# Performance work log

Measured on AMD Instinct MI355X. Metric: run time of the kernel, lower is better.

The kernel has to match this reference:

```python
import jax
import jax.numpy as jnp
import numpy as np

# --- dimensions ---
N, B, E, T = 16384, 64, 262144, 1048576   # atoms, molecules, edges, triplets
R, S = 128, 7                              # num_radial, num_spherical
A, EM, TR = 128, 256, 32                   # emb_size_atom, emb_size_edge, emb_size_trip
CRBF, C, BIL, L = 16, 16, 64, 2            # emb_size_rbf, emb_size_cbf, emb_size_bil_trip, num_blocks
NKR, DP = 128, 8                           # num_k_rbf, downprojection_size
CUTOFF, K_CUT, DK = 6.0, 0.4, 0.2


def _k_grid_np():
    ax = np.arange(-2, 3) * DK
    g = np.stack(np.meshgrid(ax, ax, ax, indexing='ij'), -1).reshape(-1, 3)
    nrm = np.linalg.norm(g, axis=1)
    return g[(nrm <= K_CUT + 1e-9) & (nrm > 1e-12)].astype(np.float32)  # [32,3]


def _k_rbf_np(kg):
    nrm = np.linalg.norm(kg, axis=1, keepdims=True)
    centers = np.linspace(0.0, K_CUT, NKR)[None, :]
    gamma = (NKR / K_CUT) ** 2
    return np.exp(-gamma * (nrm - centers) ** 2).astype(np.float32)  # [32,NKR]


def setup_inputs():
    key = jax.random.key(0)
    ks = iter(jax.random.split(key, 48))
    def nrm(shape, fan_in):
        return jax.random.normal(next(ks), shape, jnp.float32) * (fan_in ** -0.5)
    kg_np = _k_grid_np()
    apm = N // B  # atoms per molecule
    mol = jax.random.randint(next(ks), (E,), 0, B)
    inp = {
        'pos': jax.random.uniform(next(ks), (N, 3), jnp.float32) * 5.0,
        'atom_table': jax.random.normal(next(ks), (83, A), jnp.float32),
        'W_edge': nrm((2 * A + R, EM), 2 * A + R), 'b_edge': jnp.zeros((EM,), jnp.float32),
        'W_rbf3': nrm((R, CRBF), R), 'W_rbf3_E': nrm((L, CRBF, EM), CRBF),
        'W_cbf3': nrm((S, R, C), R),
        'W_ba': nrm((L, EM, EM), EM),
        'W_downtrip': nrm((L, EM, TR), EM),
        'W_bil': nrm((L, C, TR, BIL), C * TR),
        'W_up': nrm((L, BIL, EM), BIL),
        'W_res1': nrm((L, EM, EM), EM), 'W_res2': nrm((L, EM, EM), EM),
        'W_rbf_h': nrm((R, CRBF), R), 'W_h': nrm((L, CRBF, EM), CRBF),
        'W_atom': nrm((L, EM, A), EM),
        'k_grid': jnp.asarray(kg_np), 'k_rbf_values': jnp.asarray(_k_rbf_np(kg_np)),
        'W_downk': nrm((NKR, DP), NKR), 'W_kfilter': nrm((DP, A), DP),
        'W_ew': nrm((L, A, A), A),
        'W_cat': nrm((L, 2 * A + EM, EM), 2 * A + EM),
        'W_rbf_out': nrm((R, CRBF), R), 'W_oute': nrm((CRBF, EM), CRBF),
        'W_out1': nrm((EM, A), EM), 'W_out2': nrm((A, 1), A),
        'z': jax.random.randint(next(ks), (N,), 0, 83),
        'edge_src': mol * apm + jax.random.randint(next(ks), (E,), 0, apm),
        'edge_tgt': mol * apm + jax.random.randint(next(ks), (E,), 0, apm),
        'id3_ba': jax.random.randint(next(ks), (T,), 0, E),
        'id3_ca': jax.random.randint(next(ks), (T,), 0, E),
        'batch_idx': jnp.arange(N, dtype=jnp.int32) // apm,
    }
    return inp


def _legendre(x):
    # P_0..P_{S-1}(x) via recurrence
    p = [jnp.ones_like(x), x]
    for l in range(1, S - 1):
        p.append(((2 * l + 1) * x * p[-1] - l * p[-2]) / (l + 1))
    return jnp.stack(p[:S], axis=-1)  # [T,S]


def _forward(pos, atom_table, W_edge, b_edge, W_rbf3, W_rbf3_E, W_cbf3, W_ba,
             W_downtrip, W_bil, W_up, W_res1, W_res2, W_rbf_h, W_h, W_atom,
             k_grid, k_rbf_values, W_downk, W_kfilter, W_ew, W_cat,
             W_rbf_out, W_oute, W_out1, W_out2,
             z, edge_src, edge_tgt, id3_ba, id3_ca, batch_idx):
    seg = lambda x, ids, n: jax.ops.segment_sum(x, ids, num_segments=n)
    silu = jax.nn.silu
    isq2 = 2.0 ** -0.5

    # radial basis (spherical Bessel) with polynomial envelope p=5
    vec = pos[edge_src] - pos[edge_tgt]                       # [E,3]
    d = jnp.sqrt(jnp.sum(vec * vec, -1) + 1e-12)              # [E]
    ds = d / CUTOFF
    env = jnp.where(ds < 1.0, 1.0 - 21.0 * ds**5 + 35.0 * ds**6 - 15.0 * ds**7, 0.0)
    freq = jnp.arange(1, R + 1, dtype=pos.dtype) * jnp.pi
    rbf = env[:, None] * (2.0 / CUTOFF) ** 0.5 * jnp.sin(freq * ds[:, None]) / d[:, None]  # [E,R]

    # circular basis: Legendre polys of triplet angle b->a<-c, combined with rbf of edge c->a
    cos_ang = jnp.clip(jnp.sum(vec[id3_ba] * vec[id3_ca], -1) / (d[id3_ba] * d[id3_ca]), -1.0, 1.0)
    sph = _legendre(cos_ang)                                  # [T,S]
    rW = jnp.einsum('er,src->esc', rbf, W_cbf3)               # [E,S,C]
    cbf = jnp.zeros((sph.shape[0], C), pos.dtype)
    for s in range(S):  # small fixed loop over spherical order (memory-safe gather)
        cbf = cbf + sph[:, s, None] * rW[:, s, :][id3_ca]     # [T,C]

    # atom + edge embeddings
    h = atom_table[z]                                         # [N,A]
    m = silu(jnp.concatenate([h[edge_src], h[edge_tgt], rbf], -1) @ W_edge + b_edge)  # [E,EM]

    # Ewald k-space geometry and learned filter
    kdot = pos @ k_grid.T                                     # [N,K]
    cosk, sink = jnp.cos(kdot), jnp.sin(kdot)
    kf = silu(k_rbf_values @ W_downk) @ W_kfilter             # [K,A]

    for l in range(L):
        # triplet message passing: gather - bilinear with cbf - scatter
        rbf3e = (rbf @ W_rbf3) @ W_rbf3_E[l]                  # [E,EM]
        x_trip = silu((silu(m @ W_ba[l]) * rbf3e) @ W_downtrip[l])  # [E,TR]
        x_kj = x_trip[id3_ba]                                 # [T,TR]
        x3 = jnp.zeros((m.shape[0], BIL), m.dtype)
        for c in range(C):  # efficient bilinear, one cbf channel at a time
            x3 = x3 + seg(cbf[:, c, None] * x_kj, id3_ca, m.shape[0]) @ W_bil[l, c]
        m = (m + silu(x3 @ W_up[l])) * isq2
        m = (m + silu(silu(m @ W_res1[l]) @ W_res2[l])) * isq2
        # atom update: rbf-gated edge->atom scatter
        ha = seg(m * ((rbf @ W_rbf_h) @ W_h[l]), edge_tgt, h.shape[0]) @ W_atom[l]  # [N,A]
        # Ewald block: per-molecule structure factors, filtered in k-space
        sf_re = seg(cosk[:, :, None] * h[:, None, :], batch_idx, B) * kf  # [B,K,A]
        sf_im = seg(sink[:, :, None] * h[:, None, :], batch_idx, B) * kf
        ew = (jnp.einsum('nk,nka->na', cosk, sf_re[batch_idx]) +
              jnp.einsum('nk,nka->na', sink, sf_im[batch_idx]))           # [N,A]
        h = (h + silu(ha) + silu(ew @ W_ew[l])) * (3.0 ** -0.5)
        # edge refresh (concat block)
        m = silu(jnp.concatenate([h[edge_src], h[edge_tgt], m], -1) @ W_cat[l])

    # output block: rbf-gated scatter to atoms, per-molecule extensive energy
    Ea = seg(m * ((rbf @ W_rbf_out) @ W_oute), edge_tgt, h.shape[0])       # [N,EM]
    atom_e = silu(Ea @ W_out1) @ W_out2                                     # [N,1]
    return seg(atom_e[:, 0], batch_idx, B)                                  # [B]


def reference(pos, atom_table, W_edge, b_edge, W_rbf3, W_rbf3_E, W_cbf3, W_ba,
              W_downtrip, W_bil, W_up, W_res1, W_res2, W_rbf_h, W_h, W_atom,
              k_grid, k_rbf_values, W_downk, W_kfilter, W_ew, W_cat,
              W_rbf_out, W_oute, W_out1, W_out2,
              z, edge_src, edge_tgt, id3_ba, id3_ca, batch_idx):
    return _forward(pos, atom_table, W_edge, b_edge, W_rbf3, W_rbf3_E, W_cbf3, W_ba,
                    W_downtrip, W_bil, W_up, W_res1, W_res2, W_rbf_h, W_h, W_atom,
                    k_grid, k_rbf_values, W_downk, W_kfilter, W_ew, W_cat,
                    W_rbf_out, W_oute, W_out1, W_out2,
                    z, edge_src, edge_tgt, id3_ba, id3_ca, batch_idx)
```

## Files before the change

kernel.cpp:

```cpp
#include <hip/hip_runtime.h>
#include <math.h>

#define NA 16384
#define NB 64
#define NE 262144
#define NT 1048576
#define NR 128
#define DA 128
#define DEM 256
#define DTR 32
#define DC 16
#define DBIL 64
#define DNKR 128
#define DDP 8
#define NK 32
#define APM 256
#define PI_F 3.14159265358979323846f

typedef unsigned short u16;
typedef unsigned int u32;
typedef __attribute__((ext_vector_type(8))) short bf16x8;
typedef __attribute__((ext_vector_type(4))) float f32x4;

__device__ __forceinline__ float silu_f(float x){ return x / (1.0f + __expf(-x)); }
__device__ __forceinline__ float us2f(u32 u){ return __uint_as_float(u<<16); }
__device__ __forceinline__ u16 f2us(float f){
  u32 x = __float_as_uint(f);
  u32 r = x + 0x7fffu + ((x>>16)&1u);
  return (u16)(r>>16);
}
__device__ __forceinline__ void unp8(uint4 v, float* o){
  o[0]=us2f(v.x&0xffffu); o[1]=us2f(v.x>>16);
  o[2]=us2f(v.y&0xffffu); o[3]=us2f(v.y>>16);
  o[4]=us2f(v.z&0xffffu); o[5]=us2f(v.z>>16);
  o[6]=us2f(v.w&0xffffu); o[7]=us2f(v.w>>16);
}
__device__ __forceinline__ uint4 pack8(const float* v){
  uint4 r;
  r.x = (u32)f2us(v[0]) | ((u32)f2us(v[1])<<16);
  r.y = (u32)f2us(v[2]) | ((u32)f2us(v[3])<<16);
  r.z = (u32)f2us(v[4]) | ((u32)f2us(v[5])<<16);
  r.w = (u32)f2us(v[6]) | ((u32)f2us(v[7])<<16);
  return r;
}
__device__ __forceinline__ float rbf_val(float d, int r){
  float ds = d*(1.0f/6.0f);
  float env = 0.0f;
  if (ds < 1.0f){
    float p2 = ds*ds, p5 = p2*p2*ds;
    env = 1.0f - 21.0f*p5 + 35.0f*p5*ds - 15.0f*p5*p2;
  }
  return env * 0.5773502691896258f * __sinf((float)(r+1)*PI_F*ds) / d;
}

__device__ __forceinline__ bf16x8 ldsA(const u16* sA, int row, int KLD, int slot){
  int s = slot ^ (row&7);
  return *(const bf16x8*)(sA + row*KLD + s*8);
}
__device__ __forceinline__ void stSlot(u16* sA, int row, int KLD, int slot, uint4 v){
  int s = slot ^ (row&7);
  *(uint4*)(sA + row*KLD + s*8) = v;
}
__device__ __forceinline__ void stW(u16* sA, int row, int KLD, int col, u16 v){
  int s = (col>>3) ^ (row&7);
  sA[row*KLD + s*8 + (col&7)] = v;
}
__device__ __forceinline__ bf16x8 ldB(const u16* Wt, int col, int K, int koff){
  return *(const bf16x8*)(Wt + (size_t)col*K + koff);
}

__global__ void k_zero(int* __restrict__ p, int n){
  int i = blockIdx.x*256+threadIdx.x; if (i<n) p[i]=0;
}

__global__ void k_wprep(const float* __restrict__ src, u16* __restrict__ dst,
                        int K, int N, int Kpad){
  int i = blockIdx.x*256+threadIdx.x;
  if (i >= N*Kpad) return;
  int n = i / Kpad, k = i - n*Kpad;
  dst[(size_t)n*Kpad + k] = (k<K)? f2us(src[(size_t)k*N + n]) : (u16)0;
}
__global__ void k_wprep_cbf(const float* __restrict__ src, u16* __restrict__ dst){
  int i = blockIdx.x*256+threadIdx.x;
  if (i >= 112*128) return;
  int n = i>>7, k = i&127;
  int s = n>>4, c = n&15;
  dst[i] = f2us(src[s*2048 + k*16 + c]);
}

__global__ void k_geom(const float* __restrict__ pos, const int* __restrict__ src,
                       const int* __restrict__ tgt, float4* __restrict__ vecd,
                       float* __restrict__ dlen){
  int e = blockIdx.x*256+threadIdx.x;
  if (e >= NE) return;
  int s = src[e], t = tgt[e];
  float vx = pos[s*3+0]-pos[t*3+0];
  float vy = pos[s*3+1]-pos[t*3+1];
  float vz = pos[s*3+2]-pos[t*3+2];
  float d = sqrtf(vx*vx+vy*vy+vz*vz + 1e-12f);
  vecd[e] = make_float4(vx,vy,vz,1.0f/d);
  dlen[e] = d;
}

__global__ void __launch_bounds__(256)
k_rbf16(const float* __restrict__ dlen, const float* __restrict__ W1,
        const float* __restrict__ W2, const float* __restrict__ W3,
        u16* __restrict__ r16a, u16* __restrict__ r16h, u16* __restrict__ r16o){
  __shared__ float rb[4*128];
  int e0 = blockIdx.x*4;
  int tid = threadIdx.x, eg = tid>>6, lt = tid&63;
  int e = e0+eg;
  float d = dlen[e];
  rb[eg*128+lt]    = rbf_val(d, lt);
  rb[eg*128+lt+64] = rbf_val(d, lt+64);
  __syncthreads();
  if (lt < 48){
    int which = lt>>4, jj = lt&15;
    const float* W = (which==0)? W1 : (which==1)? W2 : W3;
    float acc=0.f;
    for (int r=0;r<NR;r++) acc += rb[eg*128+r]*W[r*16+jj];
    u16* o = (which==0)? r16a : (which==1)? r16h : r16o;
    o[(size_t)e*16+jj] = f2us(acc);
  }
}

__global__ void k_gather_h(const float* __restrict__ table, const int* __restrict__ z,
                           float* __restrict__ h){
  int idx = blockIdx.x*256 + threadIdx.x;
  int n = idx >> 7, a = idx & 127;
  h[idx] = table[z[n]*DA + a];
}

__global__ void k_kdot(const float* __restrict__ pos, const float* __restrict__ kg,
                       float* __restrict__ cosk, float* __restrict__ sink_){
  int idx = blockIdx.x*256+threadIdx.x;
  int n = idx>>5, k = idx&31;
  float dotv = pos[n*3]*kg[k*3]+pos[n*3+1]*kg[k*3+1]+pos[n*3+2]*kg[k*3+2];
  float s, c;
  sincosf(dotv, &s, &c);
  cosk[idx] = c; sink_[idx] = s;
}

__global__ void k_kf(const float* __restrict__ krbf, const float* __restrict__ Wd,
                     const float* __restrict__ Wf, float* __restrict__ kf){
  __shared__ float t[NK*DDP];
  int tid = threadIdx.x;
  { int k = tid>>3, d = tid&7;
    float s=0.f;
    for (int r=0;r<DNKR;r++) s += krbf[k*DNKR+r]*Wd[r*DDP+d];
    t[tid] = silu_f(s); }
  __syncthreads();
  for (int idx=tid; idx<NK*DA; idx+=256){
    int k = idx>>7, a = idx&127;
    float s=0.f;
    #pragma unroll
    for (int d=0; d<DDP; d++) s += t[k*DDP+d]*Wf[d*DA+a];
    kf[idx]=s;
  }
}

__global__ void k_count(const int* __restrict__ ids, int num, int* __restrict__ cnt){
  int i = blockIdx.x*256+threadIdx.x;
  if (i<num) atomicAdd(&cnt[ids[i]],1);
}
__global__ void k_scan1(const int* __restrict__ cnt, int n, int* __restrict__ loc,
                        int* __restrict__ part){
  __shared__ int lds[256];
  int i = blockIdx.x*256+threadIdx.x;
  int v = (i<n)?cnt[i]:0;
  lds[threadIdx.x]=v; __syncthreads();
  for (int off=1; off<256; off<<=1){
    int tv = (threadIdx.x >= (unsigned)off)? lds[threadIdx.x-off]:0;
    __syncthreads();
    lds[threadIdx.x]+=tv;
    __syncthreads();
  }
  if (i<n) loc[i] = lds[threadIdx.x]-v;
  if (threadIdx.x==255) part[blockIdx.x]=lds[255];
}
__global__ void k_scan2(int* __restrict__ part, int nparts){
  __shared__ int lds[1024];
  int tid=threadIdx.x;
  for (int i=tid;i<1024;i+=256) lds[i] = (i<nparts)? part[i] : 0;
  __syncthreads();
  if (tid==0){
    int run=0;
    for (int i=0;i<nparts;i++){ int v=lds[i]; lds[i]=run; run+=v; }
  }
  __syncthreads();
  for (int i=tid;i<1024;i+=256) if (i<nparts) part[i]=lds[i];
}
__global__ void k_scan3(const int* __restrict__ loc, const int* __restrict__ part,
                        const int* __restrict__ cnt, int n, int* __restrict__ off){
  int i = blockIdx.x*256+threadIdx.x;
  if (i<n){ int o = loc[i]+part[i>>8]; off[i]=o; if (i==n-1) off[n]=o+cnt[i]; }
}
__global__ void k_copy_int(const int* __restrict__ a, int n, int* __restrict__ b){
  int i=blockIdx.x*256+threadIdx.x; if(i<n) b[i]=a[i];
}
__global__ void k_fill(const int* __restrict__ ids, int num, int* __restrict__ cur,
                       int* __restrict__ list){
  int i = blockIdx.x*256+threadIdx.x;
  if (i<num){ int p = atomicAdd(&cur[ids[i]],1); list[p]=i; }
}
__global__ void k_fill_val(const int* __restrict__ ids, const int* __restrict__ vals,
                           int num, int* __restrict__ cur, int* __restrict__ list){
  int i = blockIdx.x*256+threadIdx.x;
  if (i<num){ int p = atomicAdd(&cur[ids[i]],1); list[p]=vals[i]; }
}


__global__ void __launch_bounds__(256)
k_edgeinit_mx(const float* __restrict__ h, const float* __restrict__ dlen,
              const u16* __restrict__ Wt, const float* __restrict__ bias,
              const int* __restrict__ src, const int* __restrict__ tgt,
              u16* __restrict__ outm){
  __shared__ u16 sA[64*256];
  int e0 = blockIdx.x*64;
  int j = threadIdx.x, lane = j&63, w = j>>6;
  int rbase = (w&1)*32, cbase = (w>>1)*128;
  int l15 = lane&15, kg = lane>>4;
  f32x4 acc[2][8];
  #pragma unroll
  for (int rt=0;rt<2;rt++)
    #pragma unroll
    for (int i=0;i<8;i++) acc[rt][i] = (f32x4){0.f,0.f,0.f,0.f};
  for (int idx=j; idx<64*32; idx+=256){
    int row = idx>>5, slot = idx&31;
    int e = e0+row;
    const float* srcp = (slot<16)? (h + (size_t)src[e]*DA + slot*8)
                                 : (h + (size_t)tgt[e]*DA + (slot-16)*8);
    float v[8];
    float4 q0 = *(const float4*)srcp, q1 = *(const float4*)(srcp+4);
    v[0]=q0.x; v[1]=q0.y; v[2]=q0.z; v[3]=q0.w;
    v[4]=q1.x; v[5]=q1.y; v[6]=q1.z; v[7]=q1.w;
    stSlot(sA, row, 256, slot, pack8(v));
  }
  __syncthreads();
  #pragma unroll 2
  for (int kc=0; kc<8; kc++){
    bf16x8 a0 = ldsA(sA, rbase+l15,    256, kc*4+kg);
    bf16x8 a1 = ldsA(sA, rbase+16+l15, 256, kc*4+kg);
    #pragma unroll
    for (int ct=0; ct<8; ct++){
      bf16x8 b = ldB(Wt, cbase+ct*16+l15, 384, kc*32+kg*8);
      acc[0][ct] = __builtin_amdgcn_mfma_f32_16x16x32_bf16(a0, b, acc[0][ct], 0,0,0);
      acc[1][ct] = __builtin_amdgcn_mfma_f32_16x16x32_bf16(a1, b, acc[1][ct], 0,0,0);
    }
  }
  __syncthreads();
  for (int idx=j; idx<64*16; idx+=256){
    int row = idx>>4, slot = idx&15;
    float dv = dlen[e0+row];
    float v[8];
    #pragma unroll
    for (int q=0;q<8;q++) v[q] = rbf_val(dv, slot*8+q);
    stSlot(sA, row, 256, slot, pack8(v));
  }
  __syncthreads();
  #pragma unroll 2
  for (int kc=8; kc<12; kc++){
    bf16x8 a0 = ldsA(sA, rbase+l15,    256, (kc-8)*4+kg);
    bf16x8 a1 = ldsA(sA, rbase+16+l15, 256, (kc-8)*4+kg);
    #pragma unroll
    for (int ct=0; ct<8; ct++){
      bf16x8 b = ldB(Wt, cbase+ct*16+l15, 384, kc*32+kg*8);
      acc[0][ct] = __builtin_amdgcn_mfma_f32_16x16x32_bf16(a0, b, acc[0][ct], 0,0,0);
      acc[1][ct] = __builtin_amdgcn_mfma_f32_16x16x32_bf16(a1, b, acc[1][ct], 0,0,0);
    }
  }
  #pragma unroll
  for (int rt=0;rt<2;rt++)
  #pragma unroll
  for (int ct=0; ct<8; ct++){
    int col = cbase + ct*16 + l15;
    float bv = bias[col];
    #pragma unroll
    for (int r=0;r<4;r++){
      int row = rbase + rt*16 + kg*4 + r;
      outm[(size_t)(e0+row)*DEM + col] = f2us(silu_f(acc[rt][ct][r] + bv));
    }
  }
}

__global__ void __launch_bounds__(256)
k_ba_dt_mx(const u16* __restrict__ m, const u16* __restrict__ WtBA,
           const u16* __restrict__ r16, const u16* __restrict__ WtR3E,
           const u16* __restrict__ WtDT, u16* __restrict__ xtrip){
  __shared__ u16 sM[32*256];
  __shared__ u16 sR[32*64];
  int e0 = blockIdx.x*32;
  int j = threadIdx.x, lane = j&63, w = j>>6;
  for (int p=j; p<32*32; p+=256){
    int row = p>>5, slot = p&31;
    uint4 v = *(const uint4*)(m + (size_t)(e0+row)*DEM + slot*8);
    stSlot(sM, row, 256, slot, v);
  }
  for (int p=j; p<32*8; p+=256){
    int row = p>>3, slot = p&7;
    uint4 v = {0u,0u,0u,0u};
    if (slot<2) v = *(const uint4*)(r16 + (size_t)(e0+row)*16 + slot*8);
    stSlot(sR, row, 64, slot, v);
  }
  __syncthreads();
  int rbase = (w&1)*16, cbase = (w>>1)*128;
  int l15 = lane&15, kg = lane>>4;
  int arow = rbase + l15;
  f32x4 accA[8], accG[8];
  #pragma unroll
  for (int i=0;i<8;i++){ accA[i]=(f32x4){0.f,0.f,0.f,0.f}; accG[i]=(f32x4){0.f,0.f,0.f,0.f}; }
  #pragma unroll 2
  for (int kc=0; kc<8; kc++){
    bf16x8 a = ldsA(sM, arow, 256, kc*4+kg);
    #pragma unroll
    for (int ct=0; ct<8; ct++){
      bf16x8 b = ldB(WtBA, cbase+ct*16+l15, 256, kc*32+kg*8);
      accA[ct] = __builtin_amdgcn_mfma_f32_16x16x32_bf16(a, b, accA[ct], 0,0,0);
    }
  }
  { bf16x8 a = ldsA(sR, arow, 64, kg);
    #pragma unroll
    for (int ct=0; ct<8; ct++){
      bf16x8 b = ldB(WtR3E, cbase+ct*16+l15, 32, kg*8);
      accG[ct] = __builtin_amdgcn_mfma_f32_16x16x32_bf16(a, b, accG[ct], 0,0,0);
    } }
  __syncthreads();
  #pragma unroll
  for (int ct=0; ct<8; ct++){
    int col = cbase + ct*16 + l15;
    #pragma unroll
    for (int r=0;r<4;r++){
      int row = rbase + kg*4 + r;
      stW(sM, row, 256, col, f2us(silu_f(accA[ct][r])*accG[ct][r]));
    }
  }
  __syncthreads();
  int rb2 = (w&1)*16, ct2 = (w>>1);
  int arow2 = rb2 + l15;
  f32x4 acc2 = (f32x4){0.f,0.f,0.f,0.f};
  #pragma unroll 2
  for (int kc=0; kc<8; kc++){
    bf16x8 a = ldsA(sM, arow2, 256, kc*4+kg);
    bf16x8 b = ldB(WtDT, ct2*16+l15, 256, kc*32+kg*8);
    acc2 = __builtin_amdgcn_mfma_f32_16x16x32_bf16(a, b, acc2, 0,0,0);
  }
  #pragma unroll
  for (int r=0;r<4;r++){
    int row = rb2 + kg*4 + r;
    int col = ct2*16 + l15;
    xtrip[(size_t)(e0+row)*DTR + col] = f2us(silu_f(acc2[r]));
  }
}

__global__ void __launch_bounds__(256)
k_trip(const int* __restrict__ ca_off, const int* __restrict__ ba_list,
       const float4* __restrict__ vecd, const float* __restrict__ dlen,
       const u16* __restrict__ WtCBF, const u16* __restrict__ xtrip,
       const u16* __restrict__ WtBIL, const u16* __restrict__ WtUP,
       u16* __restrict__ m){
  __shared__ u16 sS3[16*512];
  __shared__ u16 sRB[16*128];
  __shared__ float rWl[16*112];
  __shared__ u16 sX3[16*64];
  int e0 = blockIdx.x*16;
  int tid = threadIdx.x, lane = tid&63, w = tid>>6;
  int l15 = lane&15, kg = lane>>4;
  for (int idx=tid; idx<2048; idx+=256){
    int e = idx>>7, r = idx&127;
    stW(sRB, e, 128, r, f2us(rbf_val(dlen[e0+e], r)));
  }
  __syncthreads();
  for (int ct=w; ct<7; ct+=4){
    f32x4 acc = (f32x4){0.f,0.f,0.f,0.f};
    for (int kc=0; kc<4; kc++){
      bf16x8 a = ldsA(sRB, l15, 128, kc*4+kg);
      bf16x8 b = ldB(WtCBF, ct*16+l15, 128, kc*32+kg*8);
      acc = __builtin_amdgcn_mfma_f32_16x16x32_bf16(a, b, acc, 0,0,0);
    }
    #pragma unroll
    for (int r=0;r<4;r++)
      rWl[(kg*4+r)*112 + ct*16 + l15] = acc[r];
  }
  __syncthreads();
  int half = lane>>5, tr = lane&31;
  for (int sub=0; sub<4; sub++){
    int el = w*4+sub, e = e0+el;
    float4 vd = vecd[e];
    float a0=0.f,a1=0.f,a2=0.f,a3=0.f,a4=0.f,a5=0.f,a6=0.f;
    int beg = ca_off[e], end = ca_off[e+1];
    int cnt = end - beg;
    int c0 = (cnt+1)>>1;
    int mybeg = beg + half*c0;
    int myend = half ? end : beg+c0;
    float4 bd = make_float4(0.f,0.f,0.f,1.f);
    float xk = 0.f;
    if (mybeg<myend){
      int b0 = ba_list[mybeg];
      bd = vecd[b0];
      xk = us2f(xtrip[(size_t)b0*DTR + tr]);
    }
    for (int ti=mybeg; ti<myend; ti++){
      int bn = (ti+1<myend)? ba_list[ti+1] : 0;
      float4 bd_n = vecd[bn];
      float xk_n = us2f(xtrip[(size_t)bn*DTR + tr]);
      float x = (vd.x*bd.x + vd.y*bd.y + vd.z*bd.z)*vd.w*bd.w;
      x = fminf(1.0f, fmaxf(-1.0f, x));
      float p2 = (3.f*x*x - 1.f)*0.5f;
      float p3 = (5.f*x*p2 - 2.f*x)*(1.0f/3.0f);
      float p4 = (7.f*x*p3 - 3.f*p2)*0.25f;
      float p5 = (9.f*x*p4 - 4.f*p3)*0.2f;
      float p6 = (11.f*x*p5 - 5.f*p4)*(1.0f/6.0f);
      a0 += xk;    a1 += x*xk;  a2 += p2*xk; a3 += p3*xk;
      a4 += p4*xk; a5 += p5*xk; a6 += p6*xk;
      bd = bd_n; xk = xk_n;
    }
    a0 += __shfl_xor(a0, 32); a1 += __shfl_xor(a1, 32);
    a2 += __shfl_xor(a2, 32); a3 += __shfl_xor(a3, 32);
    a4 += __shfl_xor(a4, 32); a5 += __shfl_xor(a5, 32);
    a6 += __shfl_xor(a6, 32);
    const float* rwe = rWl + el*112;
    #pragma unroll
    for (int q=0;q<8;q++){
      int c = half*8+q;
      float s3 = rwe[c]*a0 + rwe[16+c]*a1 + rwe[32+c]*a2 + rwe[48+c]*a3
               + rwe[64+c]*a4 + rwe[80+c]*a5 + rwe[96+c]*a6;
      stW(sS3, el, 512, c*32+tr, f2us(s3));
    }
  }
  __syncthreads();
  { f32x4 acc = (f32x4){0.f,0.f,0.f,0.f};
    #pragma unroll 2
    for (int kc=0; kc<16; kc++){
      bf16x8 a = ldsA(sS3, l15, 512, kc*4+kg);
      bf16x8 b = ldB(WtBIL, w*16+l15, 512, kc*32+kg*8);
      acc = __builtin_amdgcn_mfma_f32_16x16x32_bf16(a, b, acc, 0,0,0);
    }
    #pragma unroll
    for (int r=0;r<4;r++)
      stW(sX3, kg*4+r, 64, w*16+l15, f2us(acc[r]));
  }
  __syncthreads();
  f32x4 acc2[4];
  #pragma unroll
  for (int i=0;i<4;i++) acc2[i] = (f32x4){0.f,0.f,0.f,0.f};
  for (int kc=0; kc<2; kc++){
    bf16x8 a = ldsA(sX3, l15, 64, kc*4+kg);
    #pragma unroll
    for (int ct=0; ct<4; ct++){
      bf16x8 b = ldB(WtUP, w*64+ct*16+l15, 64, kc*32+kg*8);
      acc2[ct] = __builtin_amdgcn_mfma_f32_16x16x32_bf16(a, b, acc2[ct], 0,0,0);
    }
  }
  #pragma unroll
  for (int ct=0; ct<4; ct++){
    int col = w*64 + ct*16 + l15;
    #pragma unroll
    for (int r=0;r<4;r++){
      int row = kg*4 + r;
      size_t oi = (size_t)(e0+row)*DEM + col;
      m[oi] = f2us((us2f(m[oi]) + silu_f(acc2[ct][r]))*0.7071067811865476f);
    }
  }
}

__global__ void __launch_bounds__(256)
k_res_mx(const u16* __restrict__ WtR1, const u16* __restrict__ WtR2, u16* __restrict__ m){
  __shared__ u16 sM[64*256];
  int e0 = blockIdx.x*64;
  int j = threadIdx.x, lane = j&63, w = j>>6;
  for (int p=j; p<64*32; p+=256){
    int row = p>>5, slot = p&31;
    uint4 v = *(const uint4*)(m + (size_t)(e0+row)*DEM + slot*8);
    stSlot(sM, row, 256, slot, v);
  }
  __syncthreads();
  int rbase = (w&1)*32, cbase = (w>>1)*128;
  int l15 = lane&15, kg = lane>>4;
  f32x4 acc[2][8];
  #pragma unroll
  for (int rt=0;rt<2;rt++)
    #pragma unroll
    for (int i=0;i<8;i++) acc[rt][i]=(f32x4){0.f,0.f,0.f,0.f};
  #pragma unroll 2
  for (int kc=0; kc<8; kc++){
    bf16x8 a0 = ldsA(sM, rbase+l15,    256, kc*4+kg);
    bf16x8 a1 = ldsA(sM, rbase+16+l15, 256, kc*4+kg);
    #pragma unroll
    for (int ct=0; ct<8; ct++){
      bf16x8 b = ldB(WtR1, cbase+ct*16+l15, 256, kc*32+kg*8);
      acc[0][ct] = __builtin_amdgcn_mfma_f32_16x16x32_bf16(a0, b, acc[0][ct], 0,0,0);
      acc[1][ct] = __builtin_amdgcn_mfma_f32_16x16x32_bf16(a1, b, acc[1][ct], 0,0,0);
    }
  }
  __syncthreads();
  #pragma unroll
  for (int rt=0;rt<2;rt++)
  #pragma unroll
  for (int ct=0; ct<8; ct++){
    int col = cbase + ct*16 + l15;
    #pragma unroll
    for (int r=0;r<4;r++)
      stW(sM, rbase + rt*16 + kg*4 + r, 256, col, f2us(silu_f(acc[rt][ct][r])));
  }
  __syncthreads();
  #pragma unroll
  for (int rt=0;rt<2;rt++)
    #pragma unroll
    for (int i=0;i<8;i++) acc[rt][i]=(f32x4){0.f,0.f,0.f,0.f};
  #pragma unroll 2
  for (int kc=0; kc<8; kc++){
    bf16x8 a0 = ldsA(sM, rbase+l15,    256, kc*4+kg);
    bf16x8 a1 = ldsA(sM, rbase+16+l15, 256, kc*4+kg);
    #pragma unroll
    for (int ct=0; ct<8; ct++){
      bf16x8 b = ldB(WtR2, cbase+ct*16+l15, 256, kc*32+kg*8);
      acc[0][ct] = __builtin_amdgcn_mfma_f32_16x16x32_bf16(a0, b, acc[0][ct], 0,0,0);
      acc[1][ct] = __builtin_amdgcn_mfma_f32_16x16x32_bf16(a1, b, acc[1][ct], 0,0,0);
    }
  }
  #pragma unroll
  for (int rt=0;rt<2;rt++)
  #pragma unroll
  for (int ct=0; ct<8; ct++){
    int col = cbase + ct*16 + l15;
    #pragma unroll
    for (int r=0;r<4;r++){
      int row = rbase + rt*16 + kg*4 + r;
      size_t oi = (size_t)(e0+row)*DEM + col;
      float orig = us2f(m[oi]);
      m[oi] = f2us((orig + silu_f(acc[rt][ct][r]))*0.7071067811865476f);
    }
  }
}

__global__ void __launch_bounds__(256)
k_catref_mx(const float* __restrict__ h, const u16* __restrict__ Wt,
            const int* __restrict__ src, const int* __restrict__ tgt,
            u16* __restrict__ m){
  __shared__ u16 sA[64*256];
  int e0 = blockIdx.x*64;
  int j = threadIdx.x, lane = j&63, w = j>>6;
  int rbase = (w&1)*32, cbase = (w>>1)*128;
  int l15 = lane&15, kg = lane>>4;
  f32x4 acc[2][8];
  #pragma unroll
  for (int rt=0;rt<2;rt++)
    #pragma unroll
    for (int i=0;i<8;i++) acc[rt][i]=(f32x4){0.f,0.f,0.f,0.f};
  for (int idx=j; idx<64*32; idx+=256){
    int row = idx>>5, slot = idx&31;
    int e = e0+row;
    const float* srcp = (slot<16)? (h + (size_t)src[e]*DA + slot*8)
                                 : (h + (size_t)tgt[e]*DA + (slot-16)*8);
    float v[8];
    float4 q0 = *(const float4*)srcp, q1 = *(const float4*)(srcp+4);
    v[0]=q0.x; v[1]=q0.y; v[2]=q0.z; v[3]=q0.w;
    v[4]=q1.x; v[5]=q1.y; v[6]=q1.z; v[7]=q1.w;
    stSlot(sA, row, 256, slot, pack8(v));
  }
  __syncthreads();
  #pragma unroll 2
  for (int kc=0; kc<8; kc++){
    bf16x8 a0 = ldsA(sA, rbase+l15,    256, kc*4+kg);
    bf16x8 a1 = ldsA(sA, rbase+16+l15, 256, kc*4+kg);
    #pragma unroll
    for (int ct=0; ct<8; ct++){
      bf16x8 b = ldB(Wt, cbase+ct*16+l15, 512, kc*32+kg*8);
      acc[0][ct] = __builtin_amdgcn_mfma_f32_16x16x32_bf16(a0, b, acc[0][ct], 0,0,0);
      acc[1][ct] = __builtin_amdgcn_mfma_f32_16x16x32_bf16(a1, b, acc[1][ct], 0,0,0);
    }
  }
  __syncthreads();
  for (int p=j; p<64*32; p+=256){
    int row = p>>5, slot = p&31;
    uint4 v = *(const uint4*)(m + (size_t)(e0+row)*DEM + slot*8);
    stSlot(sA, row, 256, slot, v);
  }
  __syncthreads();
  #pragma unroll 2
  for (int kc=8; kc<16; kc++){
    bf16x8 a0 = ldsA(sA, rbase+l15,    256, (kc-8)*4+kg);
    bf16x8 a1 = ldsA(sA, rbase+16+l15, 256, (kc-8)*4+kg);
    #pragma unroll
    for (int ct=0; ct<8; ct++){
      bf16x8 b = ldB(Wt, cbase+ct*16+l15, 512, kc*32+kg*8);
      acc[0][ct] = __builtin_amdgcn_mfma_f32_16x16x32_bf16(a0, b, acc[0][ct], 0,0,0);
      acc[1][ct] = __builtin_amdgcn_mfma_f32_16x16x32_bf16(a1, b, acc[1][ct], 0,0,0);
    }
  }
  __syncthreads();
  #pragma unroll
  for (int rt=0;rt<2;rt++)
  #pragma unroll
  for (int ct=0; ct<8; ct++){
    int col = cbase + ct*16 + l15;
    #pragma unroll
    for (int r=0;r<4;r++){
      int row = rbase + rt*16 + kg*4 + r;
      m[(size_t)(e0+row)*DEM + col] = f2us(silu_f(acc[rt][ct][r]));
    }
  }
}

__global__ void __launch_bounds__(256)
k_gseg(const int* __restrict__ off, const int* __restrict__ list,
       const u16* __restrict__ m, const u16* __restrict__ r16,
       const float* __restrict__ Wg, float* __restrict__ outp){
  __shared__ float sW[16*256];
  int n = blockIdx.x, j = threadIdx.x;
  for (int idx=j; idx<4096; idx+=256) sW[idx] = Wg[idx];
  __syncthreads();
  float s = 0.f;
  int beg = off[n], end = off[n+1];
  for (int ii=beg; ii<end; ii++){
    int e = list[ii];
    const uint4* rp = (const uint4*)(r16 + (size_t)e*16);
    float rv[16];
    unp8(rp[0], rv); unp8(rp[1], rv+8);
    float g = 0.f;
    #pragma unroll
    for (int i=0;i<16;i++) g += rv[i]*sW[i*256+j];
    s += us2f(m[(size_t)e*DEM + j])*g;
  }
  outp[(size_t)n*DEM + j] = s;
}

__global__ void k_sf(const float* __restrict__ cosk, const float* __restrict__ sink_,
                     const float* __restrict__ h, const float* __restrict__ kf,
                     float* __restrict__ sfre, float* __restrict__ sfim){
  int bk = blockIdx.x; int b = bk>>5, k = bk&31;
  int a = threadIdx.x;
  float sre=0.f, sim=0.f;
  int n0 = b*APM;
  for (int i=0;i<APM;i++){
    float c = cosk[(n0+i)*NK+k];
    float s = sink_[(n0+i)*NK+k];
    float hv = h[(size_t)(n0+i)*DA+a];
    sre += c*hv; sim += s*hv;
  }
  float f = kf[k*DA+a];
  sfre[(size_t)bk*DA+a] = sre*f;
  sfim[(size_t)bk*DA+a] = sim*f;
}

__global__ void k_ew(const float* __restrict__ cosk, const float* __restrict__ sink_,
                     const float* __restrict__ sfre, const float* __restrict__ sfim,
                     float* __restrict__ ew){
  int n = blockIdx.x; int a = threadIdx.x; int b = n>>8;
  float s=0.f;
  for (int k=0;k<NK;k++){
    s += cosk[n*NK+k]*sfre[(size_t)(b*NK+k)*DA+a] + sink_[n*NK+k]*sfim[(size_t)(b*NK+k)*DA+a];
  }
  ew[(size_t)n*DA+a]=s;
}

__global__ void __launch_bounds__(128)
k_hup(const float* __restrict__ hsum, const float* __restrict__ ewb,
      const float* __restrict__ Wat, const float* __restrict__ Wew,
      float* __restrict__ h){
  __shared__ float sA[16*256];
  __shared__ float sB[16*128];
  int row0 = blockIdx.x*16;
  int j = threadIdx.x;
  for (int idx=j; idx<4096; idx+=128) sA[idx] = hsum[(size_t)row0*DEM + idx];
  for (int idx=j; idx<2048; idx+=128) sB[idx] = ewb[(size_t)row0*DA + idx];
  __syncthreads();
  float a1[16], a2[16];
  #pragma unroll
  for (int i=0;i<16;i++){ a1[i]=0.f; a2[i]=0.f; }
  for (int k=0;k<256;k++){
    float w = Wat[k*DA+j];
    #pragma unroll
    for (int i=0;i<16;i++) a1[i] += sA[i*256+k]*w;
  }
  for (int k=0;k<128;k++){
    float w = Wew[k*DA+j];
    #pragma unroll
    for (int i=0;i<16;i++) a2[i] += sB[i*128+k]*w;
  }
  #pragma unroll
  for (int i=0;i<16;i++){
    size_t oi = (size_t)(row0+i)*DA + j;
    h[oi] = (h[oi] + silu_f(a1[i]) + silu_f(a2[i]))*0.5773502691896258f;
  }
}

__global__ void k_out_atom(const float* __restrict__ Ea, const float* __restrict__ W1,
                           const float* __restrict__ W2, float* __restrict__ atom_e){
  __shared__ float red[128];
  int n = blockIdx.x; int j = threadIdx.x;
  const float* row = Ea + (size_t)n*DEM;
  float s=0.f;
  for (int k=0;k<DEM;k++) s += row[k]*W1[k*DA+j];
  float v = silu_f(s)*W2[j];
  red[j]=v; __syncthreads();
  for (int st=64; st>0; st>>=1){ if (j<st) red[j]+=red[j+st]; __syncthreads(); }
  if (j==0) atom_e[n]=red[0];
}

__global__ void k_out_mol(const float* __restrict__ atom_e, float* __restrict__ out){
  __shared__ float red[256];
  int b = blockIdx.x; int t = threadIdx.x;
  red[t] = atom_e[b*APM+t]; __syncthreads();
  for (int st=128; st>0; st>>=1){ if (t<st) red[t]+=red[t+st]; __syncthreads(); }
  if (t==0) out[b]=red[0];
}

extern "C" void kernel_launch(void* const* d_in, const int* in_sizes, int n_in,
                              void* d_out, int out_size, void* d_ws, size_t ws_size,
                              hipStream_t stream){
  (void)in_sizes; (void)n_in; (void)out_size;
  const float* pos    = (const float*)d_in[0];
  const float* atab   = (const float*)d_in[1];
  const float* W_edge = (const float*)d_in[2];
  const float* b_edge = (const float*)d_in[3];
  const float* W_rbf3 = (const float*)d_in[4];
  const float* W_rbf3E= (const float*)d_in[5];
  const float* W_cbf3 = (const float*)d_in[6];
  const float* W_ba   = (const float*)d_in[7];
  const float* W_dt   = (const float*)d_in[8];
  const float* W_bil  = (const float*)d_in[9];
  const float* W_up   = (const float*)d_in[10];
  const float* W_r1   = (const float*)d_in[11];
  const float* W_r2   = (const float*)d_in[12];
  const float* W_rbfh = (const float*)d_in[13];
  const float* W_h    = (const float*)d_in[14];
  const float* W_atom = (const float*)d_in[15];
  const float* kgrid  = (const float*)d_in[16];
  const float* krbfv  = (const float*)d_in[17];
  const float* W_dk   = (const float*)d_in[18];
  const float* W_kf   = (const float*)d_in[19];
  const float* W_ewm  = (const float*)d_in[20];
  const float* W_cat  = (const float*)d_in[21];
  const float* W_rbfo = (const float*)d_in[22];
  const float* W_oute = (const float*)d_in[23];
  const float* W_o1   = (const float*)d_in[24];
  const float* W_o2   = (const float*)d_in[25];
  const int* z     = (const int*)d_in[26];
  const int* esrc  = (const int*)d_in[27];
  const int* etgt  = (const int*)d_in[28];
  const int* id3ba = (const int*)d_in[29];
  const int* id3ca = (const int*)d_in[30];
  float* out = (float*)d_out;

  char* base = (char*)d_ws;
  size_t off = 0;
  auto alloc = [&](size_t bytes)->char*{
    char* p = base + off;
    off += (bytes + 255) & ~(size_t)255;
    return p;
  };
  u16*   m     = (u16*)  alloc((size_t)NE*DEM*2);
  float4* vecd = (float4*)alloc((size_t)NE*16);
  float* dlen  = (float*)alloc((size_t)NE*4);
  u16*   r16a  = (u16*)  alloc((size_t)NE*16*2);
  u16*   r16h  = (u16*)  alloc((size_t)NE*16*2);
  u16*   r16o  = (u16*)  alloc((size_t)NE*16*2);
  float* h     = (float*)alloc((size_t)NA*DA*4);
  float* cosk  = (float*)alloc((size_t)NA*NK*4);
  float* sinkb = (float*)alloc((size_t)NA*NK*4);
  float* sfre  = (float*)alloc((size_t)NB*NK*DA*4);
  float* sfim  = (float*)alloc((size_t)NB*NK*DA*4);
  float* kf    = (float*)alloc((size_t)NK*DA*4);
  float* atome = (float*)alloc((size_t)NA*4);
  char*  scr   = alloc((size_t)24*1024*1024);
  int* tgt_off = (int*)alloc((size_t)(NA+1)*4);
  int* tgt_list= (int*)alloc((size_t)NE*4);
  int* ca_off  = (int*)alloc((size_t)(NE+1)*4);
  int* ca_list = (int*)alloc((size_t)NT*4);
  int* parts   = (int*)alloc((size_t)1024*4);
  u16* wt_edge = (u16*)alloc((size_t)256*384*2);
  u16* wt_ba   = (u16*)alloc((size_t)2*256*256*2);
  u16* wt_r3e  = (u16*)alloc((size_t)2*256*32*2);
  u16* wt_dt   = (u16*)alloc((size_t)2*32*256*2);
  u16* wt_up   = (u16*)alloc((size_t)2*256*64*2);
  u16* wt_r1   = (u16*)alloc((size_t)2*256*256*2);
  u16* wt_r2   = (u16*)alloc((size_t)2*256*256*2);
  u16* wt_cat  = (u16*)alloc((size_t)2*256*512*2);
  u16* wt_cbf  = (u16*)alloc((size_t)112*128*2);
  u16* wt_bil  = (u16*)alloc((size_t)2*64*512*2);
  size_t need = off;
  if (ws_size < need) return;

  u16*   xtrip = (u16*)scr;
  float* hsum  = (float*)scr;
  float* ewb   = (float*)(scr + (size_t)16*1024*1024);
  int* tmpi    = (int*)r16a;
  int* tgt_cnt = tmpi;
  int* tgt_loc = tmpi + NA;
  int* tgt_cur = tmpi + 2*NA;
  int* ca_cnt  = tmpi + 3*NA;
  int* ca_loc  = ca_cnt + NE;
  int* ca_cur  = ca_loc + NE;

  auto wprep = [&](const float* src, u16* dst, int K, int N, int Kpad){
    int tot = N*Kpad;
    k_wprep<<<(tot+255)/256, 256, 0, stream>>>(src, dst, K, N, Kpad);
  };
  wprep(W_edge, wt_edge, 384, 256, 384);
  k_wprep_cbf<<<(112*128+255)/256, 256, 0, stream>>>(W_cbf3, wt_cbf);
  for (int l=0; l<2; l++){
    wprep(W_ba  + (size_t)l*256*256, wt_ba  + (size_t)l*256*256, 256, 256, 256);
    wprep(W_rbf3E+(size_t)l*16*256,  wt_r3e + (size_t)l*256*32,  16,  256, 32);
    wprep(W_dt  + (size_t)l*256*32,  wt_dt  + (size_t)l*32*256,  256, 32,  256);
    wprep(W_up  + (size_t)l*64*256,  wt_up  + (size_t)l*256*64,  64,  256, 64);
    wprep(W_r1  + (size_t)l*256*256, wt_r1  + (size_t)l*256*256, 256, 256, 256);
    wprep(W_r2  + (size_t)l*256*256, wt_r2  + (size_t)l*256*256, 256, 256, 256);
    wprep(W_cat + (size_t)l*512*256, wt_cat + (size_t)l*256*512, 512, 256, 512);
    wprep(W_bil + (size_t)l*512*64,  wt_bil + (size_t)l*64*512,  512, 64,  512);
  }

  k_geom<<<NE/256, 256, 0, stream>>>(pos, esrc, etgt, vecd, dlen);

  k_zero<<<NA/256, 256, 0, stream>>>(tgt_cnt, NA);
  k_count<<<NE/256, 256, 0, stream>>>(etgt, NE, tgt_cnt);
  k_scan1<<<NA/256, 256, 0, stream>>>(tgt_cnt, NA, tgt_loc, parts);
  k_scan2<<<1, 256, 0, stream>>>(parts, NA/256);
  k_scan3<<<NA/256, 256, 0, stream>>>(tgt_loc, parts, tgt_cnt, NA, tgt_off);
  k_copy_int<<<NA/256, 256, 0, stream>>>(tgt_off, NA, tgt_cur);
  k_fill<<<NE/256, 256, 0, stream>>>(etgt, NE, tgt_cur, tgt_list);

  k_zero<<<NE/256, 256, 0, stream>>>(ca_cnt, NE);
  k_count<<<NT/256, 256, 0, stream>>>(id3ca, NT, ca_cnt);
  k_scan1<<<NE/256, 256, 0, stream>>>(ca_cnt, NE, ca_loc, parts);
  k_scan2<<<1, 256, 0, stream>>>(parts, NE/256);
  k_scan3<<<NE/256, 256, 0, stream>>>(ca_loc, parts, ca_cnt, NE, ca_off);
  k_copy_int<<<NE/256, 256, 0, stream>>>(ca_off, NE, ca_cur);
  k_fill_val<<<NT/256, 256, 0, stream>>>(id3ca, id3ba, NT, ca_cur, ca_list);

  k_rbf16<<<NE/4, 256, 0, stream>>>(dlen, W_rbf3, W_rbfh, W_rbfo, r16a, r16h, r16o);
  k_gather_h<<<NA*DA/256, 256, 0, stream>>>(atab, z, h);
  k_kdot<<<NA*NK/256, 256, 0, stream>>>(pos, kgrid, cosk, sinkb);
  k_kf<<<1, 256, 0, stream>>>(krbfv, W_dk, W_kf, kf);
  k_edgeinit_mx<<<NE/64, 256, 0, stream>>>(h, dlen, wt_edge, b_edge, esrc, etgt, m);

  for (int l=0; l<2; l++){
    k_ba_dt_mx<<<NE/32, 256, 0, stream>>>(m, wt_ba + (size_t)l*256*256,
                                          r16a, wt_r3e + (size_t)l*256*32,
                                          wt_dt + (size_t)l*32*256, xtrip);
    k_trip<<<NE/16, 256, 0, stream>>>(ca_off, ca_list, vecd, dlen, wt_cbf,
                                      xtrip, wt_bil + (size_t)l*64*512,
                                      wt_up + (size_t)l*256*64, m);
    k_res_mx<<<NE/64, 256, 0, stream>>>(wt_r1 + (size_t)l*256*256,
                                        wt_r2 + (size_t)l*256*256, m);
    k_gseg<<<NA, 256, 0, stream>>>(tgt_off, tgt_list, m, r16h, W_h + (size_t)l*16*DEM, hsum);
    k_sf<<<NB*NK, 128, 0, stream>>>(cosk, sinkb, h, kf, sfre, sfim);
    k_ew<<<NA, 128, 0, stream>>>(cosk, sinkb, sfre, sfim, ewb);
    k_hup<<<NA/16, 128, 0, stream>>>(hsum, ewb, W_atom + (size_t)l*DEM*DA,
                                     W_ewm + (size_t)l*DA*DA, h);
    k_catref_mx<<<NE/64, 256, 0, stream>>>(h, wt_cat + (size_t)l*256*512, esrc, etgt, m);
  }

  k_gseg<<<NA, 256, 0, stream>>>(tgt_off, tgt_list, m, r16o, W_oute, hsum);
  k_out_atom<<<NA, 128, 0, stream>>>(hsum, W_o1, W_o2, atome);
  k_out_mol<<<NB, 256, 0, stream>>>(atome, out);
}
```

Before: 3.891 ms.

## Renumber edges in target-sorted order so segment reductions read contiguously

Edges are permuted into target-sorted order using the tgt CSR list. Triplet indices are remapped through an inverse permutation, and all per-edge arrays are built in that order. This lets the per-atom segment sums read m and rbf rows contiguously instead of gathering through an index list, which should improve locality in k_gseg and in the triplet and catref gathers. The cost is a few extra preprocessing kernels. Edge ordering now depends on the atomic fill order, but the sums are order-invariant.

```diff
diff --git a/kernel.cpp b/kernel.cpp
--- a/kernel.cpp
+++ b/kernel.cpp
@@ -88,6 +88,28 @@
   dst[i] = f2us(src[s*2048 + k*16 + c]);
 }
 
+__global__ void k_iperm(const int* __restrict__ list, int n, int* __restrict__ iperm){
+  int i = blockIdx.x*256+threadIdx.x;
+  if (i<n) iperm[list[i]] = i;
+}
+__global__ void k_permute2(const int* __restrict__ list, const int* __restrict__ a,
+                           const int* __restrict__ b, int n,
+                           int* __restrict__ ap, int* __restrict__ bp){
+  int i = blockIdx.x*256+threadIdx.x;
+  if (i<n){ int e = list[i]; ap[i]=a[e]; bp[i]=b[e]; }
+}
+__global__ void k_count_map(const int* __restrict__ ids, const int* __restrict__ map,
+                            int num, int* __restrict__ cnt){
+  int i = blockIdx.x*256+threadIdx.x;
+  if (i<num) atomicAdd(&cnt[map[ids[i]]],1);
+}
+__global__ void k_fill_valmap(const int* __restrict__ ids, const int* __restrict__ vals,
+                              const int* __restrict__ map, int num,
+                              int* __restrict__ cur, int* __restrict__ list){
+  int i = blockIdx.x*256+threadIdx.x;
+  if (i<num){ int p = atomicAdd(&cur[map[ids[i]]],1); list[p]=map[vals[i]]; }
+}
+
 __global__ void k_geom(const float* __restrict__ pos, const int* __restrict__ src,
                        const int* __restrict__ tgt, float4* __restrict__ vecd,
                        float* __restrict__ dlen){
@@ -202,11 +224,6 @@
                        int* __restrict__ list){
   int i = blockIdx.x*256+threadIdx.x;
   if (i<num){ int p = atomicAdd(&cur[ids[i]],1); list[p]=i; }
-}
-__global__ void k_fill_val(const int* __restrict__ ids, const int* __restrict__ vals,
-                           int num, int* __restrict__ cur, int* __restrict__ list){
-  int i = blockIdx.x*256+threadIdx.x;
-  if (i<num){ int p = atomicAdd(&cur[ids[i]],1); list[p]=vals[i]; }
 }
 
 
@@ -603,17 +620,16 @@
 }
 
 __global__ void __launch_bounds__(256)
-k_gseg(const int* __restrict__ off, const int* __restrict__ list,
-       const u16* __restrict__ m, const u16* __restrict__ r16,
-       const float* __restrict__ Wg, float* __restrict__ outp){
+k_gseg_seq(const int* __restrict__ off, const u16* __restrict__ m,
+           const u16* __restrict__ r16, const float* __restrict__ Wg,
+           float* __restrict__ outp){
   __shared__ float sW[16*256];
   int n = blockIdx.x, j = threadIdx.x;
   for (int idx=j; idx<4096; idx+=256) sW[idx] = Wg[idx];
   __syncthreads();
   float s = 0.f;
   int beg = off[n], end = off[n+1];
-  for (int ii=beg; ii<end; ii++){
-    int e = list[ii];
+  for (int e=beg; e<end; e++){
     const uint4* rp = (const uint4*)(r16 + (size_t)e*16);
     float rv[16];
     unp8(rp[0], rv); unp8(rp[1], rv+8);
@@ -766,6 +782,9 @@
   char*  scr   = alloc((size_t)24*1024*1024);
   int* tgt_off = (int*)alloc((size_t)(NA+1)*4);
   int* tgt_list= (int*)alloc((size_t)NE*4);
+  int* iperm   = (int*)alloc((size_t)NE*4);
+  int* esrc_p  = (int*)alloc((size_t)NE*4);
+  int* etgt_p  = (int*)alloc((size_t)NE*4);
   int* ca_off  = (int*)alloc((size_t)(NE+1)*4);
   int* ca_list = (int*)alloc((size_t)NT*4);
   int* parts   = (int*)alloc((size_t)1024*4);
@@ -810,8 +829,6 @@
     wprep(W_bil + (size_t)l*512*64,  wt_bil + (size_t)l*64*512,  512, 64,  512);
   }
 
-  k_geom<<<NE/256, 256, 0, stream>>>(pos, esrc, etgt, vecd, dlen);
-
   k_zero<<<NA/256, 256, 0, stream>>>(tgt_cnt, NA);
   k_count<<<NE/256, 256, 0, stream>>>(etgt, NE, tgt_cnt);
   k_scan1<<<NA/256, 256, 0, stream>>>(tgt_cnt, NA, tgt_loc, parts);
@@ -819,20 +836,24 @@
   k_scan3<<<NA/256, 256, 0, stream>>>(tgt_loc, parts, tgt_cnt, NA, tgt_off);
   k_copy_int<<<NA/256, 256, 0, stream>>>(tgt_off, NA, tgt_cur);
   k_fill<<<NE/256, 256, 0, stream>>>(etgt, NE, tgt_cur, tgt_list);
+  k_iperm<<<NE/256, 256, 0, stream>>>(tgt_list, NE, iperm);
+  k_permute2<<<NE/256, 256, 0, stream>>>(tgt_list, esrc, etgt, NE, esrc_p, etgt_p);
+
+  k_geom<<<NE/256, 256, 0, stream>>>(pos, esrc_p, etgt_p, vecd, dlen);
 
   k_zero<<<NE/256, 256, 0, stream>>>(ca_cnt, NE);
-  k_count<<<NT/256, 256, 0, stream>>>(id3ca, NT, ca_cnt);
+  k_count_map<<<NT/256, 256, 0, stream>>>(id3ca, iperm, NT, ca_cnt);
   k_scan1<<<NE/256, 256, 0, stream>>>(ca_cnt, NE, ca_loc, parts);
   k_scan2<<<1, 256, 0, stream>>>(parts, NE/256);
   k_scan3<<<NE/256, 256, 0, stream>>>(ca_loc, parts, ca_cnt, NE, ca_off);
   k_copy_int<<<NE/256, 256, 0, stream>>>(ca_off, NE, ca_cur);
-  k_fill_val<<<NT/256, 256, 0, stream>>>(id3ca, id3ba, NT, ca_cur, ca_list);
+  k_fill_valmap<<<NT/256, 256, 0, stream>>>(id3ca, id3ba, iperm, NT, ca_cur, ca_list);
 
   k_rbf16<<<NE/4, 256, 0, stream>>>(dlen, W_rbf3, W_rbfh, W_rbfo, r16a, r16h, r16o);
   k_gather_h<<<NA*DA/256, 256, 0, stream>>>(atab, z, h);
   k_kdot<<<NA*NK/256, 256, 0, stream>>>(pos, kgrid, cosk, sinkb);
   k_kf<<<1, 256, 0, stream>>>(krbfv, W_dk, W_kf, kf);
-  k_edgeinit_mx<<<NE/64, 256, 0, stream>>>(h, dlen, wt_edge, b_edge, esrc, etgt, m);
+  k_edgeinit_mx<<<NE/64, 256, 0, stream>>>(h, dlen, wt_edge, b_edge, esrc_p, etgt_p, m);
 
   for (int l=0; l<2; l++){
     k_ba_dt_mx<<<NE/32, 256, 0, stream>>>(m, wt_ba + (size_t)l*256*256,
@@ -843,15 +864,15 @@
                                       wt_up + (size_t)l*256*64, m);
     k_res_mx<<<NE/64, 256, 0, stream>>>(wt_r1 + (size_t)l*256*256,
                                         wt_r2 + (size_t)l*256*256, m);
-    k_gseg<<<NA, 256, 0, stream>>>(tgt_off, tgt_list, m, r16h, W_h + (size_t)l*16*DEM, hsum);
+    k_gseg_seq<<<NA, 256, 0, stream>>>(tgt_off, m, r16h, W_h + (size_t)l*16*DEM, hsum);
     k_sf<<<NB*NK, 128, 0, stream>>>(cosk, sinkb, h, kf, sfre, sfim);
     k_ew<<<NA, 128, 0, stream>>>(cosk, sinkb, sfre, sfim, ewb);
     k_hup<<<NA/16, 128, 0, stream>>>(hsum, ewb, W_atom + (size_t)l*DEM*DA,
                                      W_ewm + (size_t)l*DA*DA, h);
-    k_catref_mx<<<NE/64, 256, 0, stream>>>(h, wt_cat + (size_t)l*256*512, esrc, etgt, m);
-  }
-
-  k_gseg<<<NA, 256, 0, stream>>>(tgt_off, tgt_list, m, r16o, W_oute, hsum);
+    k_catref_mx<<<NE/64, 256, 0, stream>>>(h, wt_cat + (size_t)l*256*512, esrc_p, etgt_p, m);
+  }
+
+  k_gseg_seq<<<NA, 256, 0, stream>>>(tgt_off, m, r16o, W_oute, hsum);
   k_out_atom<<<NA, 128, 0, stream>>>(hsum, W_o1, W_o2, atome);
   k_out_mol<<<NB, 256, 0, stream>>>(atome, out);
 }
```

Measured after the change: 3.819 ms. About the same (-1.9%).
